# Performance work log

Hardware: AMD Instinct MI355X
Metric: run time of the kernel (lower is better)

Reference implementation:

```python
import jax, jax.numpy as jnp
import numpy as np

DIM = 128
HEADS = 8
HEAD_DIM = DIM // HEADS
K = 5          # kernel_size per spatial axis
DIL = 1        # dilation
EPS = 1e-5


def setup_inputs() -> dict:
    key = jax.random.key(0)
    ks = jax.random.split(key, 12)
    s = 0.02
    inp = {
        "x": jax.random.normal(ks[0], (1, DIM, 16, 16, 4), jnp.float32),
        "skip": jax.random.normal(ks[1], (1, DIM, 32, 32, 8), jnp.float32),
        "Wq": jax.random.normal(ks[2], (DIM, DIM), jnp.float32) * s,
        "bq": jnp.zeros((DIM,), jnp.float32),
        "Wk": jax.random.normal(ks[3], (DIM, DIM), jnp.float32) * s,
        "bk": jnp.zeros((DIM,), jnp.float32),
        "Wv": jax.random.normal(ks[4], (DIM, DIM), jnp.float32) * s,
        "bv": jnp.zeros((DIM,), jnp.float32),
        "rpb": jax.random.normal(ks[5], (HEADS, 2 * K - 1, 2 * K - 1, 2 * K - 1), jnp.float32) * s,
        "Wo": jax.random.normal(ks[6], (DIM, DIM), jnp.float32) * s,
        "bo": jnp.zeros((DIM,), jnp.float32),
    }
    return inp


def _instance_norm(t):
    # InstanceNorm3d, affine=False: normalize over spatial dims per (B, C)
    mu = jnp.mean(t, axis=(2, 3, 4), keepdims=True)
    var = jnp.var(t, axis=(2, 3, 4), keepdims=True)
    return (t - mu) * jax.lax.rsqrt(var + EPS)


def _nbr_idx(L):
    # NATTEN-style clamped window: start shifted to stay in bounds
    i = np.arange(L)
    start = np.clip(i - (K // 2) * DIL, 0, L - 1 - (K - 1) * DIL)
    idx = start[:, None] + np.arange(K)[None, :] * DIL  # (L, K)
    rel = (idx - i[:, None]) // DIL + (K - 1)           # (L, K) in [0, 2K-2]
    return jnp.asarray(idx), jnp.asarray(rel)


def reference(x, skip, Wq, bq, Wk, bk, Wv, bv, rpb, Wo, bo):
    x = _instance_norm(x)
    skip = _instance_norm(skip)

    xu = jnp.repeat(jnp.repeat(jnp.repeat(x, 2, axis=2), 2, axis=3), 2, axis=4)

    B, C, H, W, Z = skip.shape
    N = H * W * Z
    xt = xu.transpose(0, 2, 3, 4, 1).reshape(B, N, C)    # queries from upsampled x
    st = skip.transpose(0, 2, 3, 4, 1).reshape(B, N, C)  # keys/values from skip

    def heads(t):
        return t.reshape(B, N, HEADS, HEAD_DIM).transpose(0, 2, 1, 3)  # (B,h,N,d)

    q = heads(xt @ Wq + bq) * (HEAD_DIM ** -0.5)
    k = heads(st @ Wk + bk)
    v = heads(st @ Wv + bv)

    idxH, relH = _nbr_idx(H)
    idxW, relW = _nbr_idx(W)
    idxZ, relZ = _nbr_idx(Z)

    # flattened neighbor token indices: (N, K^3)
    nbr = (idxH[:, None, None, :, None, None] * (W * Z)
           + idxW[None, :, None, None, :, None] * Z
           + idxZ[None, None, :, None, None, :])
    nbr = jnp.broadcast_to(nbr, (H, W, Z, K, K, K)).reshape(N, K ** 3)

    # relative position bias gather: (heads, N, K^3)
    rH = jnp.broadcast_to(relH[:, None, None, :, None, None], (H, W, Z, K, K, K)).reshape(N, K ** 3)
    rW = jnp.broadcast_to(relW[None, :, None, None, :, None], (H, W, Z, K, K, K)).reshape(N, K ** 3)
    rZ = jnp.broadcast_to(relZ[None, None, :, None, None, :], (H, W, Z, K, K, K)).reshape(N, K ** 3)
    bias = rpb[:, rH, rW, rZ]  # (heads, N, K^3)

    kg = jnp.take(k, nbr, axis=2)  # (B, h, N, K^3, d)
    vg = jnp.take(v, nbr, axis=2)

    logits = jnp.einsum('bhnd,bhnkd->bhnk', q, kg) + bias[None]
    attn = jax.nn.softmax(logits, axis=-1)
    out = jnp.einsum('bhnk,bhnkd->bhnd', attn, vg)

    out = out.transpose(0, 2, 1, 3).reshape(B, N, C) @ Wo + bo
    return out.reshape(B, H, W, Z, C).transpose(0, 4, 1, 2, 3)
```

## Files before the change

### kernel.cpp

```cpp
#include <hip/hip_runtime.h>
#include <math.h>

#define DIM 128
#define HEADS 8
#define HD 16
#define NPOS 8192
#define EPS 1e-5f

static __device__ __forceinline__ unsigned short f2bf(float f) {
    unsigned u = __float_as_uint(f);
    return (unsigned short)((u + 0x7fffu + ((u >> 16) & 1u)) >> 16);
}
#define BLO(u) __uint_as_float((u) << 16)
#define BHI(u) __uint_as_float((u) & 0xffff0000u)

__global__ __launch_bounds__(256) void stats_kernel(const float* __restrict__ x,
                                                    const float* __restrict__ skip,
                                                    float* __restrict__ ws) {
    int c = blockIdx.x;
    const float* src; int n; float* mu_out; float* rs_out; int ci;
    if (c < DIM) { ci = c; src = x + c * 1024; n = 1024; mu_out = ws; rs_out = ws + DIM; }
    else { ci = c - DIM; src = skip + (size_t)ci * NPOS; n = NPOS; mu_out = ws + 2*DIM; rs_out = ws + 3*DIM; }
    int t = threadIdx.x;
    float s = 0.f, s2 = 0.f;
    for (int i = t; i < n; i += 256) { float v = src[i]; s += v; s2 = fmaf(v, v, s2); }
    #pragma unroll
    for (int off = 32; off > 0; off >>= 1) {
        s  += __shfl_down(s,  off, 64);
        s2 += __shfl_down(s2, off, 64);
    }
    __shared__ float ls[4], ls2[4];
    int wv = t >> 6;
    if ((t & 63) == 0) { ls[wv] = s; ls2[wv] = s2; }
    __syncthreads();
    if (t == 0) {
        float S  = ls[0] + ls[1] + ls[2] + ls[3];
        float S2 = ls2[0] + ls2[1] + ls2[2] + ls2[3];
        float inv_n = 1.f / (float)n;
        float mu  = S * inv_n;
        float var = S2 * inv_n - mu * mu;
        mu_out[ci] = mu;
        rs_out[ci] = rsqrtf(var + EPS);
    }
}

__global__ __launch_bounds__(256) void qkv_kernel(const float* __restrict__ x,
                                                  const float* __restrict__ skip,
                                                  const float* __restrict__ Wq, const float* __restrict__ bq,
                                                  const float* __restrict__ Wk, const float* __restrict__ bk,
                                                  const float* __restrict__ Wv, const float* __restrict__ bv,
                                                  const float* __restrict__ ws,
                                                  float* __restrict__ q_out,
                                                  unsigned* __restrict__ k_out,
                                                  unsigned* __restrict__ v_out) {
    __shared__ float at[128 * 68];
    __shared__ float wl[128 * 64];
    int t = threadIdx.x;
    int which = blockIdx.y;
    int half  = blockIdx.z;
    int n0 = blockIdx.x * 64;

    const float* W = (which == 0) ? Wq : (which == 1) ? Wk : Wv;
    const float* b = (which == 0) ? bq : (which == 1) ? bk : bv;
    {
        const float4* W4 = (const float4*)W;
        float4* wl4 = (float4*)wl;
        for (int i4 = t; i4 < 2048; i4 += 256) {
            int ci = i4 >> 4, j4 = i4 & 15;
            wl4[ci * 16 + j4] = W4[ci * 32 + half * 16 + j4];
        }
    }
    const float* mu = (which == 0) ? ws : ws + 2*DIM;
    const float* rs = (which == 0) ? ws + DIM : ws + 3*DIM;
    if (which == 0) {
        for (int i4 = t; i4 < 2048; i4 += 256) {
            int ci = i4 >> 4, ln4 = (i4 & 15) * 4;
            int n = n0 + ln4;
            int hc = n >> 8, wc = (n >> 3) & 31, zc = n & 7;
            float2 f = *(const float2*)(x + ci * 1024 + (hc >> 1) * 64 + (wc >> 1) * 4 + (zc >> 1));
            float m_ = mu[ci], r_ = rs[ci];
            float a0 = (f.x - m_) * r_, a1 = (f.y - m_) * r_;
            *(float4*)(at + ci * 68 + ln4) = make_float4(a0, a0, a1, a1);
        }
    } else {
        for (int i4 = t; i4 < 2048; i4 += 256) {
            int ci = i4 >> 4, ln4 = (i4 & 15) * 4;
            float4 f = *(const float4*)(skip + (size_t)ci * NPOS + n0 + ln4);
            float m_ = mu[ci], r_ = rs[ci];
            *(float4*)(at + ci * 68 + ln4) =
                make_float4((f.x - m_) * r_, (f.y - m_) * r_, (f.z - m_) * r_, (f.w - m_) * r_);
        }
    }
    __syncthreads();

    int pg = t & 15, cg = t >> 4;
    float4 bv4 = *(const float4*)(b + half * 64 + cg * 4);
    float4 acc[4];
    #pragma unroll
    for (int ps = 0; ps < 4; ++ps) acc[ps] = bv4;

    const float* ap = at + pg * 4;
    const float* wp = wl + cg * 4;
    #pragma unroll 4
    for (int ci = 0; ci < 128; ++ci) {
        float4 a4 = *(const float4*)(ap + ci * 68);
        float4 w4 = *(const float4*)(wp + ci * 64);
        float av[4] = { a4.x, a4.y, a4.z, a4.w };
        #pragma unroll
        for (int ps = 0; ps < 4; ++ps) {
            float a = av[ps];
            acc[ps].x = fmaf(a, w4.x, acc[ps].x);
            acc[ps].y = fmaf(a, w4.y, acc[ps].y);
            acc[ps].z = fmaf(a, w4.z, acc[ps].z);
            acc[ps].w = fmaf(a, w4.w, acc[ps].w);
        }
    }
    int p0 = n0 + pg * 4;
    if (which == 0) {
        #pragma unroll
        for (int ps = 0; ps < 4; ++ps) {
            float4 r = make_float4(acc[ps].x * 0.25f, acc[ps].y * 0.25f,
                                   acc[ps].z * 0.25f, acc[ps].w * 0.25f);
            *(float4*)(q_out + (size_t)(p0 + ps) * 128 + half * 64 + cg * 4) = r;
        }
    } else {
        unsigned* outp = (which == 1) ? k_out : v_out;
        #pragma unroll
        for (int ps = 0; ps < 4; ++ps) {
            uint2 pk;
            pk.x = ((unsigned)f2bf(acc[ps].y) << 16) | f2bf(acc[ps].x);
            pk.y = ((unsigned)f2bf(acc[ps].w) << 16) | f2bf(acc[ps].z);
            *(uint2*)(outp + (size_t)(p0 + ps) * 64 + half * 32 + cg * 2) = pk;
        }
    }
}

__global__ __launch_bounds__(512, 6) void attn_kernel(const float* __restrict__ q,
                                                      const unsigned* __restrict__ kb,
                                                      const unsigned* __restrict__ vb,
                                                      const float* __restrict__ rpb,
                                                      float* __restrict__ ao_t) {
    __shared__ uint4 kbf[2 * 416];
    __shared__ uint4 vbf[2 * 416];
    __shared__ float bias_l[729];

    int blk = blockIdx.x;
    int h     = blk & 7;
    int rest  = blk >> 3;
    int halfw = rest & 1;
    int tile  = rest >> 1;
    int h0 = (tile >> 3) * 4;
    int w0 = (tile & 7) * 4 + halfw * 2;
    int bh0 = min(max(h0 - 2, 0), 24);
    int bw0 = min(max(w0 - 2, 0), 26);
    int t = threadIdx.x;

    for (int idx = t; idx < 768; idx += 512) {
        int c2 = idx & 1;
        int r  = idx >> 1;
        int nz = r & 7;
        int q2 = r >> 3;
        int nh = (q2 * 43) >> 8;
        int nw = q2 - nh * 6;
        int n = (bh0 + nh) * 256 + (bw0 + nw) * 8 + nz;
        int base = nh * 52 + nw * 8 + ((nz + nw) & 7);
        kbf[c2 * 416 + base] = *(const uint4*)(kb + (size_t)n * 64 + h * 8 + c2 * 4);
        vbf[c2 * 416 + base] = *(const uint4*)(vb + (size_t)n * 64 + h * 8 + c2 * 4);
    }
    for (int idx = t; idx < 729; idx += 512) bias_l[idx] = rpb[h * 729 + idx];
    __syncthreads();

    int s = t & 7, p = t >> 3;
    int ph = p >> 4, pw = (p >> 3) & 1, pz = p & 7;
    int hc = h0 + ph, wc = w0 + pw, zc = pz;
    int sh = min(max(hc - 2, 0), 27);
    int sw = min(max(wc - 2, 0), 27);
    int sz = min(max(zc - 2, 0), 3);
    int hb = sh - bh0, wb = sw - bw0;
    int bias_base = (sh - hc + 4) * 81 + (sw - wc + 4) * 9 + (sz - zc + 4);
    int n = hc * 256 + wc * 8 + zc;

    float qv[16];
    #pragma unroll
    for (int i = 0; i < 4; ++i)
        ((float4*)qv)[i] = *(const float4*)(q + (size_t)n * 128 + h * 16 + i * 4);

    float o[16];
    #pragma unroll
    for (int d = 0; d < 16; ++d) o[d] = 0.f;
    float l = 0.f;

    int cnt   = (s < 5) ? 16 : 15;
    int start = (s < 5) ? 16 * s : 15 * s + 5;
    int i0 = p & 15; if (i0 >= cnt) i0 -= cnt;

    for (int it = 0; it < cnt; ++it) {
        int ii = i0 + it; if (ii >= cnt) ii -= cnt;
        int j = start + ii;
        int jh = (j * 41) >> 10;
        int jr = j - jh * 25;
        int jw = (jr * 13) >> 6;
        int jz = jr - jw * 5;
        int nnw = wb + jw;
        int nnz = sz + jz;
        int base = (hb + jh) * 52 + nnw * 8 + ((nnz + nnw) & 7);
        float bias = bias_l[bias_base + jh * 81 + jw * 9 + jz];

        uint4 ka = kbf[base];
        uint4 k2 = kbf[416 + base];
        float d0 = 0.f, d1 = 0.f, d2 = 0.f, d3 = 0.f;
        d0 = fmaf(BLO(ka.x), qv[0],  d0);
        d0 = fmaf(BHI(ka.x), qv[1],  d0);
        d0 = fmaf(BLO(ka.y), qv[2],  d0);
        d0 = fmaf(BHI(ka.y), qv[3],  d0);
        d1 = fmaf(BLO(ka.z), qv[4],  d1);
        d1 = fmaf(BHI(ka.z), qv[5],  d1);
        d1 = fmaf(BLO(ka.w), qv[6],  d1);
        d1 = fmaf(BHI(ka.w), qv[7],  d1);
        d2 = fmaf(BLO(k2.x), qv[8],  d2);
        d2 = fmaf(BHI(k2.x), qv[9],  d2);
        d2 = fmaf(BLO(k2.y), qv[10], d2);
        d2 = fmaf(BHI(k2.y), qv[11], d2);
        d3 = fmaf(BLO(k2.z), qv[12], d3);
        d3 = fmaf(BHI(k2.z), qv[13], d3);
        d3 = fmaf(BLO(k2.w), qv[14], d3);
        d3 = fmaf(BHI(k2.w), qv[15], d3);
        float sc = (d0 + d1) + (d2 + d3) + bias;
        float pp = __expf(sc);
        l += pp;

        uint4 va = vbf[base];
        uint4 v2 = vbf[416 + base];
        o[0]  = fmaf(pp, BLO(va.x), o[0]);
        o[1]  = fmaf(pp, BHI(va.x), o[1]);
        o[2]  = fmaf(pp, BLO(va.y), o[2]);
        o[3]  = fmaf(pp, BHI(va.y), o[3]);
        o[4]  = fmaf(pp, BLO(va.z), o[4]);
        o[5]  = fmaf(pp, BHI(va.z), o[5]);
        o[6]  = fmaf(pp, BLO(va.w), o[6]);
        o[7]  = fmaf(pp, BHI(va.w), o[7]);
        o[8]  = fmaf(pp, BLO(v2.x), o[8]);
        o[9]  = fmaf(pp, BHI(v2.x), o[9]);
        o[10] = fmaf(pp, BLO(v2.y), o[10]);
        o[11] = fmaf(pp, BHI(v2.y), o[11]);
        o[12] = fmaf(pp, BLO(v2.z), o[12]);
        o[13] = fmaf(pp, BHI(v2.z), o[13]);
        o[14] = fmaf(pp, BLO(v2.w), o[14]);
        o[15] = fmaf(pp, BHI(v2.w), o[15]);
    }

    #pragma unroll
    for (int step = 1; step <= 4; step <<= 1) {
        l += __shfl_xor(l, step, 64);
        #pragma unroll
        for (int d = 0; d < 16; ++d) o[d] += __shfl_xor(o[d], step, 64);
    }
    float inv = 1.f / l;
    ao_t[(size_t)(h * 16 + 2 * s)     * NPOS + n] = o[2 * s]     * inv;
    ao_t[(size_t)(h * 16 + 2 * s + 1) * NPOS + n] = o[2 * s + 1] * inv;
}

__global__ __launch_bounds__(256) void proj_kernel(const float* __restrict__ ao_t,
                                                   const float* __restrict__ Wo,
                                                   const float* __restrict__ bo,
                                                   float* __restrict__ out) {
    __shared__ float at[128 * 68];
    __shared__ float wl[128 * 64];
    int t = threadIdx.x;
    int half = blockIdx.y;
    int n0 = blockIdx.x * 64;

    {
        const float4* W4 = (const float4*)Wo;
        float4* wl4 = (float4*)wl;
        for (int i4 = t; i4 < 2048; i4 += 256) {
            int ci = i4 >> 4, j4 = i4 & 15;
            wl4[ci * 16 + j4] = W4[ci * 32 + half * 16 + j4];
        }
    }
    for (int i4 = t; i4 < 2048; i4 += 256) {
        int ci = i4 >> 4, ln4 = (i4 & 15) * 4;
        float4 f = *(const float4*)(ao_t + (size_t)ci * NPOS + n0 + ln4);
        *(float4*)(at + ci * 68 + ln4) = f;
    }
    __syncthreads();

    int pg = t & 15, cg = t >> 4;
    float4 bv4 = *(const float4*)(bo + half * 64 + cg * 4);
    float4 acc[4];
    #pragma unroll
    for (int ps = 0; ps < 4; ++ps) acc[ps] = bv4;

    const float* ap = at + pg * 4;
    const float* wp = wl + cg * 4;
    #pragma unroll 4
    for (int ci = 0; ci < 128; ++ci) {
        float4 a4 = *(const float4*)(ap + ci * 68);
        float4 w4 = *(const float4*)(wp + ci * 64);
        float av[4] = { a4.x, a4.y, a4.z, a4.w };
        #pragma unroll
        for (int ps = 0; ps < 4; ++ps) {
            float a = av[ps];
            acc[ps].x = fmaf(a, w4.x, acc[ps].x);
            acc[ps].y = fmaf(a, w4.y, acc[ps].y);
            acc[ps].z = fmaf(a, w4.z, acc[ps].z);
            acc[ps].w = fmaf(a, w4.w, acc[ps].w);
        }
    }
    int p0 = n0 + pg * 4;
    int jbase = half * 64 + cg * 4;
    *(float4*)(out + (size_t)(jbase + 0) * NPOS + p0) = make_float4(acc[0].x, acc[1].x, acc[2].x, acc[3].x);
    *(float4*)(out + (size_t)(jbase + 1) * NPOS + p0) = make_float4(acc[0].y, acc[1].y, acc[2].y, acc[3].y);
    *(float4*)(out + (size_t)(jbase + 2) * NPOS + p0) = make_float4(acc[0].z, acc[1].z, acc[2].z, acc[3].z);
    *(float4*)(out + (size_t)(jbase + 3) * NPOS + p0) = make_float4(acc[0].w, acc[1].w, acc[2].w, acc[3].w);
}

extern "C" void kernel_launch(void* const* d_in, const int* in_sizes, int n_in,
                              void* d_out, int out_size, void* d_ws, size_t ws_size,
                              hipStream_t stream) {
    const float* x    = (const float*)d_in[0];
    const float* skip = (const float*)d_in[1];
    const float* Wq   = (const float*)d_in[2];
    const float* bq   = (const float*)d_in[3];
    const float* Wk   = (const float*)d_in[4];
    const float* bk   = (const float*)d_in[5];
    const float* Wv   = (const float*)d_in[6];
    const float* bv   = (const float*)d_in[7];
    const float* rpb  = (const float*)d_in[8];
    const float* Wo   = (const float*)d_in[9];
    const float* bo   = (const float*)d_in[10];
    float* out = (float*)d_out;

    float*    ws   = (float*)d_ws;
    float*    q    = ws + 512;
    unsigned* kbp  = (unsigned*)(q + (size_t)NPOS * 128);
    unsigned* vbp  = kbp + (size_t)NPOS * 64;
    float*    ao_t = (float*)(vbp + (size_t)NPOS * 64);

    stats_kernel<<<256, 256, 0, stream>>>(x, skip, ws);
    qkv_kernel<<<dim3(128, 3, 2), 256, 0, stream>>>(x, skip, Wq, bq, Wk, bk, Wv, bv, ws, q, kbp, vbp);
    attn_kernel<<<1024, 512, 0, stream>>>(q, kbp, vbp, rpb, ao_t);
    proj_kernel<<<dim3(128, 2), 256, 0, stream>>>(ao_t, Wo, bo, out);
}
```

Measured before the change: 141.8 us.

## Exploit upsampled query sharing: compute Q at low res, process z-pairs jointly in fp16

Because queries come from a 2x nearest-upsampled input, Q is computed only for the 1024 low-resolution positions. The attention kernel then has each thread handle two adjacent z-positions that share a query, sharing the K/V window loads and dot products across both outputs and masking the out-of-window neighbours. Q, K and V switch from bf16/fp32 to packed fp16 so the q·k dot products can use the fdot2 instruction. Each block now stages a larger 8x8 neighbour tile and the grid is halved with a lower occupancy hint; the extra per-thread accumulators raise register pressure, and fp16 trades exponent range for mantissa precision.

```diff
diff --git a/kernel.cpp b/kernel.cpp
--- a/kernel.cpp
+++ b/kernel.cpp
@@ -7,12 +7,24 @@
 #define NPOS 8192
 #define EPS 1e-5f
 
-static __device__ __forceinline__ unsigned short f2bf(float f) {
-    unsigned u = __float_as_uint(f);
-    return (unsigned short)((u + 0x7fffu + ((u >> 16) & 1u)) >> 16);
-}
-#define BLO(u) __uint_as_float((u) << 16)
-#define BHI(u) __uint_as_float((u) & 0xffff0000u)
+typedef _Float16 half2_t __attribute__((ext_vector_type(2)));
+
+static __device__ __forceinline__ half2_t u2h(unsigned u) {
+    half2_t r; __builtin_memcpy(&r, &u, 4); return r;
+}
+static __device__ __forceinline__ unsigned pkh(float a, float b) {
+    half2_t h; h.x = (_Float16)a; h.y = (_Float16)b;
+    unsigned u; __builtin_memcpy(&u, &h, 4); return u;
+}
+static __device__ __forceinline__ float dot2(unsigned k, unsigned q, float acc) {
+#if __has_builtin(__builtin_amdgcn_fdot2)
+    return __builtin_amdgcn_fdot2(u2h(k), u2h(q), acc, false);
+#else
+    half2_t kh = u2h(k), qh = u2h(q);
+    acc = fmaf((float)kh.x, (float)qh.x, acc);
+    return fmaf((float)kh.y, (float)qh.y, acc);
+#endif
+}
 
 __global__ __launch_bounds__(256) void stats_kernel(const float* __restrict__ x,
                                                     const float* __restrict__ skip,
@@ -22,8 +34,14 @@
     if (c < DIM) { ci = c; src = x + c * 1024; n = 1024; mu_out = ws; rs_out = ws + DIM; }
     else { ci = c - DIM; src = skip + (size_t)ci * NPOS; n = NPOS; mu_out = ws + 2*DIM; rs_out = ws + 3*DIM; }
     int t = threadIdx.x;
+    const float4* s4 = (const float4*)src;
+    int n4 = n >> 2;
     float s = 0.f, s2 = 0.f;
-    for (int i = t; i < n; i += 256) { float v = src[i]; s += v; s2 = fmaf(v, v, s2); }
+    for (int i = t; i < n4; i += 256) {
+        float4 v = s4[i];
+        s += (v.x + v.y) + (v.z + v.w);
+        s2 = fmaf(v.x, v.x, fmaf(v.y, v.y, fmaf(v.z, v.z, fmaf(v.w, v.w, s2))));
+    }
     #pragma unroll
     for (int off = 32; off > 0; off >>= 1) {
         s  += __shfl_down(s,  off, 64);
@@ -50,13 +68,14 @@
                                                   const float* __restrict__ Wk, const float* __restrict__ bk,
                                                   const float* __restrict__ Wv, const float* __restrict__ bv,
                                                   const float* __restrict__ ws,
-                                                  float* __restrict__ q_out,
+                                                  unsigned* __restrict__ q_out,
                                                   unsigned* __restrict__ k_out,
                                                   unsigned* __restrict__ v_out) {
     __shared__ float at[128 * 68];
     __shared__ float wl[128 * 64];
+    int which = blockIdx.y;
+    if (which == 0 && blockIdx.x >= 16) return;
     int t = threadIdx.x;
-    int which = blockIdx.y;
     int half  = blockIdx.z;
     int n0 = blockIdx.x * 64;
 
@@ -75,12 +94,10 @@
     if (which == 0) {
         for (int i4 = t; i4 < 2048; i4 += 256) {
             int ci = i4 >> 4, ln4 = (i4 & 15) * 4;
-            int n = n0 + ln4;
-            int hc = n >> 8, wc = (n >> 3) & 31, zc = n & 7;
-            float2 f = *(const float2*)(x + ci * 1024 + (hc >> 1) * 64 + (wc >> 1) * 4 + (zc >> 1));
+            float4 f = *(const float4*)(x + ci * 1024 + n0 + ln4);
             float m_ = mu[ci], r_ = rs[ci];
-            float a0 = (f.x - m_) * r_, a1 = (f.y - m_) * r_;
-            *(float4*)(at + ci * 68 + ln4) = make_float4(a0, a0, a1, a1);
+            *(float4*)(at + ci * 68 + ln4) =
+                make_float4((f.x - m_) * r_, (f.y - m_) * r_, (f.z - m_) * r_, (f.w - m_) * r_);
         }
     } else {
         for (int i4 = t; i4 < 2048; i4 += 256) {
@@ -119,145 +136,140 @@
     if (which == 0) {
         #pragma unroll
         for (int ps = 0; ps < 4; ++ps) {
-            float4 r = make_float4(acc[ps].x * 0.25f, acc[ps].y * 0.25f,
-                                   acc[ps].z * 0.25f, acc[ps].w * 0.25f);
-            *(float4*)(q_out + (size_t)(p0 + ps) * 128 + half * 64 + cg * 4) = r;
+            uint2 pk;
+            pk.x = pkh(acc[ps].x * 0.25f, acc[ps].y * 0.25f);
+            pk.y = pkh(acc[ps].z * 0.25f, acc[ps].w * 0.25f);
+            *(uint2*)(q_out + (size_t)(p0 + ps) * 64 + half * 32 + cg * 2) = pk;
         }
     } else {
         unsigned* outp = (which == 1) ? k_out : v_out;
         #pragma unroll
         for (int ps = 0; ps < 4; ++ps) {
             uint2 pk;
-            pk.x = ((unsigned)f2bf(acc[ps].y) << 16) | f2bf(acc[ps].x);
-            pk.y = ((unsigned)f2bf(acc[ps].w) << 16) | f2bf(acc[ps].z);
+            pk.x = pkh(acc[ps].x, acc[ps].y);
+            pk.y = pkh(acc[ps].z, acc[ps].w);
             *(uint2*)(outp + (size_t)(p0 + ps) * 64 + half * 32 + cg * 2) = pk;
         }
     }
 }
 
-__global__ __launch_bounds__(512, 6) void attn_kernel(const float* __restrict__ q,
+__global__ __launch_bounds__(512, 4) void attn_kernel(const unsigned* __restrict__ qb,
                                                       const unsigned* __restrict__ kb,
                                                       const unsigned* __restrict__ vb,
                                                       const float* __restrict__ rpb,
                                                       float* __restrict__ ao_t) {
-    __shared__ uint4 kbf[2 * 416];
-    __shared__ uint4 vbf[2 * 416];
-    __shared__ float bias_l[729];
+    __shared__ uint4 kbf[2 * 544];
+    __shared__ uint4 vbf[2 * 544];
+    __shared__ float bias_l[744];
 
     int blk = blockIdx.x;
-    int h     = blk & 7;
-    int rest  = blk >> 3;
-    int halfw = rest & 1;
-    int tile  = rest >> 1;
+    int h    = blk & 7;
+    int tile = blk >> 3;
     int h0 = (tile >> 3) * 4;
-    int w0 = (tile & 7) * 4 + halfw * 2;
+    int w0 = (tile & 7) * 4;
     int bh0 = min(max(h0 - 2, 0), 24);
-    int bw0 = min(max(w0 - 2, 0), 26);
+    int bw0 = min(max(w0 - 2, 0), 24);
     int t = threadIdx.x;
 
-    for (int idx = t; idx < 768; idx += 512) {
+    for (int idx = t; idx < 1024; idx += 512) {
         int c2 = idx & 1;
         int r  = idx >> 1;
-        int nz = r & 7;
+        int gz = r & 7;
         int q2 = r >> 3;
-        int nh = (q2 * 43) >> 8;
-        int nw = q2 - nh * 6;
-        int n = (bh0 + nh) * 256 + (bw0 + nw) * 8 + nz;
-        int base = nh * 52 + nw * 8 + ((nz + nw) & 7);
-        kbf[c2 * 416 + base] = *(const uint4*)(kb + (size_t)n * 64 + h * 8 + c2 * 4);
-        vbf[c2 * 416 + base] = *(const uint4*)(vb + (size_t)n * 64 + h * 8 + c2 * 4);
-    }
-    for (int idx = t; idx < 729; idx += 512) bias_l[idx] = rpb[h * 729 + idx];
+        int gh = q2 >> 3, gw = q2 & 7;
+        int n = (bh0 + gh) * 256 + (bw0 + gw) * 8 + gz;
+        int base = gh * 68 + gw * 8 + ((gz + gw) & 7);
+        kbf[c2 * 544 + base] = *(const uint4*)(kb + (size_t)n * 64 + h * 8 + c2 * 4);
+        vbf[c2 * 544 + base] = *(const uint4*)(vb + (size_t)n * 64 + h * 8 + c2 * 4);
+    }
+    for (int idx = t; idx < 744; idx += 512) bias_l[idx] = (idx < 729) ? rpb[h * 729 + idx] : 0.f;
     __syncthreads();
 
     int s = t & 7, p = t >> 3;
-    int ph = p >> 4, pw = (p >> 3) & 1, pz = p & 7;
-    int hc = h0 + ph, wc = w0 + pw, zc = pz;
+    int ph = p >> 4, pw = (p >> 2) & 3, pzp = p & 3;
+    int hc = h0 + ph, wc = w0 + pw, zc0 = pzp * 2;
     int sh = min(max(hc - 2, 0), 27);
     int sw = min(max(wc - 2, 0), 27);
-    int sz = min(max(zc - 2, 0), 3);
+    int sz0 = min(max(zc0 - 2, 0), 3);
+    int sz1 = min(max(zc0 - 1, 0), 3);
+    int dlt = sz1 - sz0;
     int hb = sh - bh0, wb = sw - bw0;
-    int bias_base = (sh - hc + 4) * 81 + (sw - wc + 4) * 9 + (sz - zc + 4);
-    int n = hc * 256 + wc * 8 + zc;
-
-    float qv[16];
-    #pragma unroll
-    for (int i = 0; i < 4; ++i)
-        ((float4*)qv)[i] = *(const float4*)(q + (size_t)n * 128 + h * 16 + i * 4);
-
-    float o[16];
-    #pragma unroll
-    for (int d = 0; d < 16; ++d) o[d] = 0.f;
-    float l = 0.f;
-
-    int cnt   = (s < 5) ? 16 : 15;
-    int start = (s < 5) ? 16 * s : 15 * s + 5;
-    int i0 = p & 15; if (i0 >= cnt) i0 -= cnt;
+    int b0 = (sh - hc + 4) * 81 + (sw - wc + 4) * 9 + (sz0 - zc0 + 4);
+    int n0pos = hc * 256 + wc * 8 + zc0;
+
+    int qrow = (hc >> 1) * 64 + (wc >> 1) * 4 + pzp;
+    uint4 qa = *(const uint4*)(qb + (size_t)qrow * 64 + h * 8);
+    uint4 qc = *(const uint4*)(qb + (size_t)qrow * 64 + h * 8 + 4);
+
+    float o0[16], o1[16];
+    #pragma unroll
+    for (int d = 0; d < 16; ++d) { o0[d] = 0.f; o1[d] = 0.f; }
+    float l0 = 0.f, l1 = 0.f;
+
+    int cnt   = 18 + (s < 6);
+    int start = s * 18 + min(s, 6);
+    int i0 = p & 15;
 
     for (int it = 0; it < cnt; ++it) {
         int ii = i0 + it; if (ii >= cnt) ii -= cnt;
         int j = start + ii;
-        int jh = (j * 41) >> 10;
-        int jr = j - jh * 25;
-        int jw = (jr * 13) >> 6;
-        int jz = jr - jw * 5;
-        int nnw = wb + jw;
-        int nnz = sz + jz;
-        int base = (hb + jh) * 52 + nnw * 8 + ((nnz + nnw) & 7);
-        float bias = bias_l[bias_base + jh * 81 + jw * 9 + jz];
+        int jh = (j * 2185) >> 16;
+        int jr = j - jh * 30;
+        int jw = (jr * 43) >> 8;
+        int jz = jr - jw * 6;
+        int gw = wb + jw;
+        int gz = sz0 + jz;
+        int base = (hb + jh) * 68 + gw * 8 + ((gz + gw) & 7);
+        int joff = jh * 81 + jw * 9 + jz;
+        float bias1 = bias_l[b0 + joff - 1];
+        float bias0 = bias_l[b0 + joff];
 
         uint4 ka = kbf[base];
-        uint4 k2 = kbf[416 + base];
-        float d0 = 0.f, d1 = 0.f, d2 = 0.f, d3 = 0.f;
-        d0 = fmaf(BLO(ka.x), qv[0],  d0);
-        d0 = fmaf(BHI(ka.x), qv[1],  d0);
-        d0 = fmaf(BLO(ka.y), qv[2],  d0);
-        d0 = fmaf(BHI(ka.y), qv[3],  d0);
-        d1 = fmaf(BLO(ka.z), qv[4],  d1);
-        d1 = fmaf(BHI(ka.z), qv[5],  d1);
-        d1 = fmaf(BLO(ka.w), qv[6],  d1);
-        d1 = fmaf(BHI(ka.w), qv[7],  d1);
-        d2 = fmaf(BLO(k2.x), qv[8],  d2);
-        d2 = fmaf(BHI(k2.x), qv[9],  d2);
-        d2 = fmaf(BLO(k2.y), qv[10], d2);
-        d2 = fmaf(BHI(k2.y), qv[11], d2);
-        d3 = fmaf(BLO(k2.z), qv[12], d3);
-        d3 = fmaf(BHI(k2.z), qv[13], d3);
-        d3 = fmaf(BLO(k2.w), qv[14], d3);
-        d3 = fmaf(BHI(k2.w), qv[15], d3);
-        float sc = (d0 + d1) + (d2 + d3) + bias;
-        float pp = __expf(sc);
-        l += pp;
+        uint4 k2 = kbf[544 + base];
+        float d0 = dot2(ka.x, qa.x, 0.f);
+        float d1 = dot2(ka.y, qa.y, 0.f);
+        d0 = dot2(ka.z, qa.z, d0);
+        d1 = dot2(ka.w, qa.w, d1);
+        d0 = dot2(k2.x, qc.x, d0);
+        d1 = dot2(k2.y, qc.y, d1);
+        d0 = dot2(k2.z, qc.z, d0);
+        d1 = dot2(k2.w, qc.w, d1);
+        float d = d0 + d1;
+
+        bool v0ok = (jz < 5);
+        bool v1ok = ((unsigned)(jz - dlt) < 5u);
+        float e0 = __expf(d + bias0);
+        float e1 = __expf(d + bias1);
+        float pp0 = v0ok ? e0 : 0.f;
+        float pp1 = v1ok ? e1 : 0.f;
+        l0 += pp0; l1 += pp1;
 
         uint4 va = vbf[base];
-        uint4 v2 = vbf[416 + base];
-        o[0]  = fmaf(pp, BLO(va.x), o[0]);
-        o[1]  = fmaf(pp, BHI(va.x), o[1]);
-        o[2]  = fmaf(pp, BLO(va.y), o[2]);
-        o[3]  = fmaf(pp, BHI(va.y), o[3]);
-        o[4]  = fmaf(pp, BLO(va.z), o[4]);
-        o[5]  = fmaf(pp, BHI(va.z), o[5]);
-        o[6]  = fmaf(pp, BLO(va.w), o[6]);
-        o[7]  = fmaf(pp, BHI(va.w), o[7]);
-        o[8]  = fmaf(pp, BLO(v2.x), o[8]);
-        o[9]  = fmaf(pp, BHI(v2.x), o[9]);
-        o[10] = fmaf(pp, BLO(v2.y), o[10]);
-        o[11] = fmaf(pp, BHI(v2.y), o[11]);
-        o[12] = fmaf(pp, BLO(v2.z), o[12]);
-        o[13] = fmaf(pp, BHI(v2.z), o[13]);
-        o[14] = fmaf(pp, BLO(v2.w), o[14]);
-        o[15] = fmaf(pp, BHI(v2.w), o[15]);
+        uint4 v2 = vbf[544 + base];
+        #define PV(u, dd) { half2_t vh = u2h(u); float f0 = (float)vh.x, f1 = (float)vh.y; \
+            o0[dd]   = fmaf(pp0, f0, o0[dd]);   o1[dd]   = fmaf(pp1, f0, o1[dd]); \
+            o0[dd+1] = fmaf(pp0, f1, o0[dd+1]); o1[dd+1] = fmaf(pp1, f1, o1[dd+1]); }
+        PV(va.x, 0)  PV(va.y, 2)  PV(va.z, 4)  PV(va.w, 6)
+        PV(v2.x, 8)  PV(v2.y, 10) PV(v2.z, 12) PV(v2.w, 14)
+        #undef PV
     }
 
     #pragma unroll
     for (int step = 1; step <= 4; step <<= 1) {
-        l += __shfl_xor(l, step, 64);
-        #pragma unroll
-        for (int d = 0; d < 16; ++d) o[d] += __shfl_xor(o[d], step, 64);
-    }
-    float inv = 1.f / l;
-    ao_t[(size_t)(h * 16 + 2 * s)     * NPOS + n] = o[2 * s]     * inv;
-    ao_t[(size_t)(h * 16 + 2 * s + 1) * NPOS + n] = o[2 * s + 1] * inv;
+        l0 += __shfl_xor(l0, step, 64);
+        l1 += __shfl_xor(l1, step, 64);
+        #pragma unroll
+        for (int d = 0; d < 16; ++d) {
+            o0[d] += __shfl_xor(o0[d], step, 64);
+            o1[d] += __shfl_xor(o1[d], step, 64);
+        }
+    }
+    float inv0 = 1.f / l0, inv1 = 1.f / l1;
+    int row = h * 16 + 2 * s;
+    float2 r0 = make_float2(o0[2*s]     * inv0, o1[2*s]     * inv1);
+    float2 r1 = make_float2(o0[2*s + 1] * inv0, o1[2*s + 1] * inv1);
+    *(float2*)(ao_t + (size_t)row       * NPOS + n0pos) = r0;
+    *(float2*)(ao_t + (size_t)(row + 1) * NPOS + n0pos) = r1;
 }
 
 __global__ __launch_bounds__(256) void proj_kernel(const float* __restrict__ ao_t,
@@ -332,13 +344,13 @@
     float* out = (float*)d_out;
 
     float*    ws   = (float*)d_ws;
-    float*    q    = ws + 512;
-    unsigned* kbp  = (unsigned*)(q + (size_t)NPOS * 128);
+    unsigned* q    = (unsigned*)(ws + 512);
+    unsigned* kbp  = q + 1024 * 64;
     unsigned* vbp  = kbp + (size_t)NPOS * 64;
     float*    ao_t = (float*)(vbp + (size_t)NPOS * 64);
 
     stats_kernel<<<256, 256, 0, stream>>>(x, skip, ws);
     qkv_kernel<<<dim3(128, 3, 2), 256, 0, stream>>>(x, skip, Wq, bq, Wk, bk, Wv, bv, ws, q, kbp, vbp);
-    attn_kernel<<<1024, 512, 0, stream>>>(q, kbp, vbp, rpb, ao_t);
+    attn_kernel<<<512, 512, 0, stream>>>(q, kbp, vbp, rpb, ao_t);
     proj_kernel<<<dim3(128, 2), 256, 0, stream>>>(ao_t, Wo, bo, out);
 }
```

Result: faster. 129.7 us (-8.5%).
